# Kernel optimization log

Measured on AMD Instinct MI355X. Metric: run time of the kernel, lower is better.

## Reference

```python
import jax, jax.numpy as jnp
import numpy as np

GH = 256       # GRU hidden size
VOCAB = 1000
MAX_EP = 150
NPREV = NCURR = NNEXT = 64


def _gru_scan(emb, h0, wih, whh, bih, bhh):
    # torch nn.GRU single-layer math, scanned over the token axis
    H = h0.shape[0]
    def step(h, x_t):
        gi = wih @ x_t + bih            # [3H]
        gh = whh @ h + bhh              # [3H]
        r = jax.nn.sigmoid(gi[:H] + gh[:H])
        z = jax.nn.sigmoid(gi[H:2 * H] + gh[H:2 * H])
        n = jnp.tanh(gi[2 * H:] + r * gh[2 * H:])
        hn = (1.0 - z) * n + z * h
        return hn, hn
    _, hs = jax.lax.scan(step, h0, emb)
    return hs                            # [L, H]


def _conv(x, w, b, s):
    y = jax.lax.conv_general_dilated(x, w, (s, s), 'VALID',
                                     dimension_numbers=('NCHW', 'OIHW', 'NCHW'))
    return y + b[None, :, None, None]


def setup_inputs():
    key = jax.random.key(0)
    ks = jax.random.split(key, 48)
    f32 = jnp.float32
    def W(i, shape, s=0.05):
        return (jax.random.normal(ks[i], shape) * s).astype(f32)
    inp = dict(
        x=jax.random.normal(ks[0], (1, 3, 124, 124), f32),
        hx=jax.random.normal(ks[1], (1, 256), f32),
        cx=jax.random.normal(ks[2], (1, 256), f32),
        conv1_w=W(3, (128, 3, 8, 8)), conv1_b=jnp.zeros((128,), f32),
        conv2_w=W(4, (64, 128, 4, 4)), conv2_b=jnp.zeros((64,), f32),
        conv3_w=W(5, (64, 64, 4, 4)), conv3_b=jnp.zeros((64,), f32),
        emb_w=W(6, (VOCAB, 32), 1.0),
        gru_f_wih=W(7, (3 * GH, 32)), gru_f_whh=W(8, (3 * GH, GH)),
        gru_f_bih=jnp.zeros((3 * GH,), f32), gru_f_bhh=jnp.zeros((3 * GH,), f32),
        gru_b_wih=W(9, (3 * GH, 32)), gru_b_whh=W(10, (3 * GH, GH)),
        gru_b_bih=jnp.zeros((3 * GH,), f32), gru_b_bhh=jnp.zeros((3 * GH,), f32),
        time_emb_w=W(11, (MAX_EP + 1, 32), 1.0),
        temp_emb_w=W(12, (2, 32), 1.0),
        img_emb_w=W(13, (256, 64 * 6 * 6)), img_emb_b=jnp.zeros((256,), f32),
        attn_key_w=W(14, (256, 256 * 3)), attn_key_b=jnp.zeros((256,), f32),
        bilinear_A=W(15, (1, 256, 544)), bilinear_b=jnp.zeros((1,), f32),
        reduce_w=W(16, (128, 544)), reduce_b=jnp.zeros((128,), f32),
        gate_w=W(17, (64, 640)), gate_b=jnp.zeros((64,), f32),
        lin_w=W(18, (256, 64 * 6 * 6)), lin_b=jnp.zeros((256,), f32),
        lstm_wih=W(19, (1024, 256)), lstm_whh=W(20, (1024, 256)),
        lstm_bih=jnp.zeros((1024,), f32), lstm_bhh=jnp.zeros((1024,), f32),
        critic_w=W(21, (1, 288)), critic_b=jnp.zeros((1,), f32),
        actor_w=W(22, (4, 288)), actor_b=jnp.zeros((4,), f32),
        prev_inst=jax.random.randint(ks[23], (1, NPREV), 0, VOCAB),
        curr_inst=jax.random.randint(ks[24], (1, NCURR), 0, VOCAB),
        next_inst=jax.random.randint(ks[25], (1, NNEXT), 0, VOCAB),
        tx=jax.random.randint(ks[26], (1,), 0, MAX_EP + 1),
    )
    return inp


def reference(x, hx, cx, conv1_w, conv1_b, conv2_w, conv2_b, conv3_w, conv3_b,
              emb_w, gru_f_wih, gru_f_whh, gru_f_bih, gru_f_bhh,
              gru_b_wih, gru_b_whh, gru_b_bih, gru_b_bhh,
              time_emb_w, temp_emb_w, img_emb_w, img_emb_b,
              attn_key_w, attn_key_b, bilinear_A, bilinear_b,
              reduce_w, reduce_b, gate_w, gate_b, lin_w, lin_b,
              lstm_wih, lstm_whh, lstm_bih, lstm_bhh,
              critic_w, critic_b, actor_w, actor_b,
              prev_inst, curr_inst, next_inst, tx):
    np_, nc, nn_ = prev_inst.shape[1], curr_inst.shape[1], next_inst.shape[1]
    all_inst = jnp.concatenate([prev_inst, curr_inst, next_inst], axis=1)[0]  # [L]
    L = all_inst.shape[0]

    # CNN encoder
    h = jax.nn.relu(_conv(x, conv1_w, conv1_b, 4))
    h = jax.nn.relu(_conv(h, conv2_w, conv2_b, 2))
    x_img = jax.nn.relu(_conv(h, conv3_w, conv3_b, 2))       # [1,64,6,6]

    # token-looped GRUs -> single lax.scan each (note: original runs gru_b
    # over the SAME forward order then reverses the hidden list; replicated)
    emb = emb_w[all_inst]                                    # [L,32]
    h0 = jnp.zeros((GH,), emb.dtype)
    hs_f = _gru_scan(emb, h0, gru_f_wih, gru_f_whh, gru_f_bih, gru_f_bhh)
    hs_b = _gru_scan(emb, h0, gru_b_wih, gru_b_whh, gru_b_bih, gru_b_bhh)[::-1]
    curr_instr_rep = jnp.concatenate([hs_f[np_ + nc - 1], hs_b[np_]])[None]  # [1,512]
    ir_f = jnp.concatenate([hs_f[:np_], hs_f[L - nn_:]], axis=0)             # [M,256]
    ir_b = jnp.concatenate([hs_b[:np_], hs_b[L - nn_:]], axis=0)
    temp_tok = jnp.concatenate([jnp.zeros((np_,), jnp.int32), jnp.ones((nn_,), jnp.int32)])
    instr_rep = jnp.concatenate([ir_f, ir_b, temp_emb_w[temp_tok]], axis=1)  # [M,544]

    # bilinear attention over prev/next token states
    image_emb = x_img.reshape(1, -1) @ img_emb_w.T + img_emb_b               # [1,256]
    attn_key = jnp.concatenate([curr_instr_rep, image_emb], 1) @ attn_key_w.T + attn_key_b
    scores = jnp.einsum('k,okv,mv->mo', attn_key[0], bilinear_A, instr_rep) + bilinear_b  # [M,1]
    w = jax.nn.softmax(scores, axis=0)
    instr_sum = (instr_rep * w).sum(0, keepdims=True)                        # [1,544]

    # gating of image features
    gating = instr_sum @ reduce_w.T + reduce_b                               # [1,128]
    gate_key = jax.nn.sigmoid(jnp.concatenate([curr_instr_rep, gating], 1) @ gate_w.T + gate_b)  # [1,64]
    xg = (x_img * gate_key[:, :, None, None]).reshape(1, -1)
    z = jax.nn.relu(xg @ lin_w.T + lin_b)                                    # [1,256]

    # LSTMCell (torch gate order i,f,g,o)
    gates = z @ lstm_wih.T + lstm_bih + hx @ lstm_whh.T + lstm_bhh           # [1,1024]
    i, f, g, o = jnp.split(gates, 4, axis=1)
    cx2 = jax.nn.sigmoid(f) * cx + jax.nn.sigmoid(i) * jnp.tanh(g)
    hx2 = jax.nn.sigmoid(o) * jnp.tanh(cx2)

    feat = jnp.concatenate([hx2, time_emb_w[tx].reshape(-1, 32)], axis=1)    # [1,288]
    critic = feat @ critic_w.T + critic_b                                    # [1,1]
    actor = feat @ actor_w.T + actor_b                                       # [1,4]
    return critic, actor, hx2, cx2
```

## Files before the change

kernel.cpp:

```cpp
#include <hip/hip_runtime.h>
#include <hip/hip_bf16.h>

__device__ __forceinline__ float bf2f(unsigned short u) {
    unsigned int v = ((unsigned int)u) << 16;
    return __builtin_bit_cast(float, v);
}
__device__ __forceinline__ float sigm(float x) { return 1.0f / (1.0f + expf(-x)); }
__device__ __forceinline__ float san(float v) {
    return (v == v && fabsf(v) < 1e20f) ? v : 12345.0f;
}
__device__ __forceinline__ void wrout(void* out, int i, float v, int f32out) {
    if (f32out) ((float*)out)[i] = v;
    else ((__hip_bfloat16*)out)[i] = __float2bfloat16(v);
}
__device__ __forceinline__ int dot4(int a, int b, int c) {
#if __has_builtin(__builtin_amdgcn_sdot4)
    return __builtin_amdgcn_sdot4(a, b, c, false);
#else
    int d;
    asm("v_dot4_i32_i8 %0, %1, %2, %3" : "=v"(d) : "v"(a), "v"(b), "v"(c));
    return d;
#endif
}
__device__ __forceinline__ float fexp2(float x) {
#if __has_builtin(__builtin_amdgcn_exp2f)
    return __builtin_amdgcn_exp2f(x);
#else
    return exp2f(x);
#endif
}
__device__ __forceinline__ float frcp(float x) {
#if __has_builtin(__builtin_amdgcn_rcpf)
    return __builtin_amdgcn_rcpf(x);
#else
    return 1.0f / x;
#endif
}
__device__ __forceinline__ float fsigm(float x) {
    return frcp(1.0f + fexp2(x * -1.44269504f));
}
__device__ __forceinline__ float ftanh(float x) {
    float t = fexp2(x * 2.88539008f);
    return 1.0f - 2.0f * frcp(t + 1.0f);
}
__device__ __forceinline__ float wave_red(float acc) {
#pragma unroll
    for (int off = 32; off >= 1; off >>= 1) acc += __shfl_down(acc, off);
    return acc;
}
__device__ __forceinline__ int dpp_xor1(int a) {
    return __builtin_amdgcn_mov_dpp(a, 0xB1, 0xF, 0xF, true);
}
__device__ __forceinline__ int dpp_xor2(int a) {
    return __builtin_amdgcn_mov_dpp(a, 0x4E, 0xF, 0xF, true);
}

struct CanonArgs {
    const void* ptr[40];
    int start[41];
    int size[40];
};

__global__ void k_flag1000(void* out) {
    if (threadIdx.x == 0) ((unsigned int*)out)[0] = 0x447A0000u;
}

__global__ void k_detect_tokens(const void* x, int nx,
                                const int* __restrict__ prev, const int* __restrict__ curr,
                                const int* __restrict__ nxt, const int* __restrict__ tx,
                                float* __restrict__ flags, int* __restrict__ toks) {
    __shared__ float sm[256];
    __shared__ int sInt64;
    int tid = threadIdx.x;
    const unsigned short* xs = (const unsigned short*)x;
    float mx = 0.0f;
    for (int i = tid; i < nx; i += 256) {
        float f = bf2f(xs[i]);
        float a = (f == f) ? fabsf(f) : 1e30f;
        mx = fmaxf(mx, a);
    }
    sm[tid] = mx;
    __syncthreads();
    for (int s = 128; s >= 1; s >>= 1) {
        if (tid < s) sm[tid] = fmaxf(sm[tid], sm[tid + s]);
        __syncthreads();
    }
    if (tid == 0) {
        flags[0] = (sm[0] > 100.0f) ? 1.0f : 0.0f;
        int anyOdd = 0;
        for (int k = 0; k < 32; ++k) anyOdd |= curr[2 * k + 1];
        int i64 = (anyOdd == 0) ? 1 : 0;
        flags[1] = (float)i64;
        sInt64 = i64;
    }
    __syncthreads();
    int stride = sInt64 ? 2 : 1;
    if (tid < 192) {
        const int* src = (tid < 64) ? prev : ((tid < 128) ? curr : nxt);
        int v = src[(tid & 63) * stride];
        toks[tid] = min(max(v, 0), 999);
    }
    if (tid == 0) toks[192] = min(max(tx[0], 0), 150);
}

__global__ void k_convert(CanonArgs a, const float* __restrict__ flags,
                          float* __restrict__ C) {
    int base = blockIdx.x << 10;
    int t = 0;
    while (t < 39 && base >= a.start[t + 1]) ++t;
    int local = base - a.start[t] + (threadIdx.x << 2);
    int sz = a.size[t];
    float4 v = make_float4(0.0f, 0.0f, 0.0f, 0.0f);
    int f32in = (flags[0] != 0.0f);
    if (local + 3 < sz) {
        if (f32in) {
            v = *(const float4*)((const float*)a.ptr[t] + local);
        } else {
            uint2 u = *(const uint2*)((const unsigned short*)a.ptr[t] + local);
            v.x = bf2f((unsigned short)(u.x & 0xffff));
            v.y = bf2f((unsigned short)(u.x >> 16));
            v.z = bf2f((unsigned short)(u.y & 0xffff));
            v.w = bf2f((unsigned short)(u.y >> 16));
        }
    } else if (local < sz) {
        float tmp[4] = {0.0f, 0.0f, 0.0f, 0.0f};
        for (int q = 0; q < 4 && local + q < sz; ++q) {
            if (f32in) tmp[q] = ((const float*)a.ptr[t])[local + q];
            else tmp[q] = bf2f(((const unsigned short*)a.ptr[t])[local + q]);
        }
        v = make_float4(tmp[0], tmp[1], tmp[2], tmp[3]);
    }
    *(float4*)(C + base + (threadIdx.x << 2)) = v;
}

__global__ void k_conv1(const float* __restrict__ x, const float* __restrict__ w,
                        const float* __restrict__ b, float* __restrict__ out) {
    int idx = blockIdx.x * 256 + threadIdx.x;
    int oc = idx / 900;
    int rem = idx - oc * 900;
    int oh = rem / 30;
    int ow = rem - oh * 30;
    float acc = b[oc];
    for (int ic = 0; ic < 3; ++ic) {
        int xb = ic * 15376 + (oh * 4) * 124 + ow * 4;
        int wb = oc * 192 + ic * 64;
#pragma unroll
        for (int kh = 0; kh < 8; ++kh) {
            const float2* xr = (const float2*)(x + xb + kh * 124);
            const float2* wr = (const float2*)(w + wb + kh * 8);
#pragma unroll
            for (int p = 0; p < 4; ++p) {
                float2 xv = xr[p];
                float2 wv = wr[p];
                acc += xv.x * wv.x + xv.y * wv.y;
            }
        }
    }
    out[idx] = fmaxf(acc, 0.0f);
}

__global__ void k_conv2(const float* __restrict__ in, const float* __restrict__ w,
                        const float* __restrict__ b, float* __restrict__ out) {
    int wid = (blockIdx.x * 256 + threadIdx.x) >> 6;
    int lane = threadIdx.x & 63;
    int oc = wid / 196;
    int rem = wid - oc * 196;
    int oh = rem / 14, ow = rem - oh * 14;
    float acc = 0.0f;
#pragma unroll 8
    for (int i = 0; i < 32; ++i) {
        int e = lane + (i << 6);
        int ic = e >> 4, k = e & 15, kh = k >> 2, kw = k & 3;
        acc += in[ic * 900 + (oh * 2 + kh) * 30 + ow * 2 + kw] * w[oc * 2048 + e];
    }
    acc = wave_red(acc);
    if (lane == 0) out[wid] = fmaxf(acc + b[oc], 0.0f);
}

__global__ void k_conv3(const float* __restrict__ in, const float* __restrict__ w,
                        const float* __restrict__ b, float* __restrict__ out) {
    int wid = (blockIdx.x * 256 + threadIdx.x) >> 6;
    int lane = threadIdx.x & 63;
    int oc = wid / 36;
    int rem = wid - oc * 36;
    int oh = rem / 6, ow = rem - oh * 6;
    float acc = 0.0f;
#pragma unroll
    for (int i = 0; i < 16; ++i) {
        int e = lane + (i << 6);
        int ic = e >> 4, k = e & 15, kh = k >> 2, kw = k & 3;
        acc += in[ic * 196 + (oh * 2 + kh) * 14 + ow * 2 + kw] * w[oc * 1024 + e];
    }
    acc = wave_red(acc);
    if (lane == 0) out[wid] = fmaxf(acc + b[oc], 0.0f);
}

__global__ void k_imgemb(const float* __restrict__ ximg, const float* __restrict__ w,
                         const float* __restrict__ b, float* __restrict__ out) {
    int j = blockIdx.x;
    int t = threadIdx.x;
    const float* wr = w + j * 2304;
    float acc = 0.0f;
    for (int k = t; k < 2304; k += 64) acc += wr[k] * ximg[k];
    acc = wave_red(acc);
    if (t == 0) out[j] = acc + b[j];
}

__global__ void k_gi(const int* __restrict__ toks, const float* __restrict__ emb,
                     const float* __restrict__ wih_f, const float* __restrict__ bih_f,
                     const float* __restrict__ bhh_f,
                     const float* __restrict__ wih_b, const float* __restrict__ bih_b,
                     const float* __restrict__ bhh_b,
                     float* __restrict__ gi) {
    int t = blockIdx.y;
    int gru = blockIdx.z;
    int j = blockIdx.x * 256 + threadIdx.x;
    __shared__ float e[32];
    int tok = toks[t];
    if (threadIdx.x < 32) e[threadIdx.x] = emb[tok * 32 + threadIdx.x];
    __syncthreads();
    const float* wih = gru ? wih_b : wih_f;
    const float* bih = gru ? bih_b : bih_f;
    const float* bhh = gru ? bhh_b : bhh_f;
    const float2* wr = (const float2*)(wih + j * 32);
    float acc = bih[j] + ((j < 512) ? bhh[j] : 0.0f);
#pragma unroll
    for (int k = 0; k < 16; ++k) {
        float2 wv = wr[k];
        acc += wv.x * e[2 * k] + wv.y * e[2 * k + 1];
    }
    gi[(gru * 192 + t) * 768 + j] = acc;
}

__global__ __launch_bounds__(512, 1) void k_gru(
    const float* __restrict__ whh_f, const float* __restrict__ bhh_f,
    const float* __restrict__ whh_b, const float* __restrict__ bhh_b,
    const float* __restrict__ gi, float* __restrict__ hs) {
    __shared__ unsigned int hq[2][72];

    int gru = blockIdx.x;
    const float* whh = gru ? whh_b : whh_f;
    const float* bhh = gru ? bhh_b : bhh_f;
    const float* gib = gi + gru * 192 * 768;
    float* hso = hs + gru * 192 * 256;

    int t = threadIdx.x;
    int c = t & 3;
    int g = t >> 2;
    int j0 = g * 2;
    int d = c & 1;
    int jme = j0 + d;

    int wq[6][16];
    float inv6[6];
#pragma unroll
    for (int rl = 0; rl < 6; ++rl) {
        int sect = rl >> 1, dd = rl & 1;
        int row = sect * 256 + j0 + dd;
        const float4* src4 = (const float4*)(whh + row * 256 + c * 64);
        float mx = 0.0f;
#pragma unroll
        for (int q = 0; q < 16; ++q) {
            float4 f = src4[q];
            mx = fmaxf(mx, fmaxf(fmaxf(fabsf(f.x), fabsf(f.y)),
                                 fmaxf(fabsf(f.z), fabsf(f.w))));
        }
        mx = fmaxf(mx, __shfl_xor(mx, 1));
        mx = fmaxf(mx, __shfl_xor(mx, 2));
        float scale = 127.0f / fmaxf(mx, 1e-20f);
        inv6[rl] = mx * (1.0f / (127.0f * 127.0f));
#pragma unroll
        for (int q = 0; q < 16; ++q) {
            float4 f = src4[q];
            int p0 = (int)rintf(f.x * scale);
            int p1 = (int)rintf(f.y * scale);
            int p2 = (int)rintf(f.z * scale);
            int p3 = (int)rintf(f.w * scale);
            wq[rl][q] = (p0 & 0xff) | ((p1 & 0xff) << 8) | ((p2 & 0xff) << 16) | (p3 << 24);
        }
    }
    float invR = d ? inv6[1] : inv6[0];
    float invZ = d ? inv6[3] : inv6[2];
    float invN = d ? inv6[5] : inv6[4];
    float bhhn = bhh[512 + jme];

    if (t < 144) ((unsigned int*)hq)[t] = 0u;
    __syncthreads();

    float hprev = 0.0f;
    float cr0 = gib[jme],       cz0 = gib[256 + jme],       cn0 = gib[512 + jme];
    float cr1 = gib[768 + jme], cz1 = gib[1024 + jme],      cn1 = gib[1280 + jme];

    auto step = [&](const unsigned int* hbuf, unsigned int* hnxt, int S,
                    float gr, float gz, float gn) {
        const uint4* hp = (const uint4*)(hbuf + c * 16);
        uint4 hv0 = hp[0], hv1 = hp[1], hv2 = hp[2], hv3 = hp[3];
        int acc[6] = {0, 0, 0, 0, 0, 0};
#pragma unroll
        for (int rl = 0; rl < 6; ++rl) {
            acc[rl] = dot4(wq[rl][0],  (int)hv0.x, acc[rl]);
            acc[rl] = dot4(wq[rl][1],  (int)hv0.y, acc[rl]);
            acc[rl] = dot4(wq[rl][2],  (int)hv0.z, acc[rl]);
            acc[rl] = dot4(wq[rl][3],  (int)hv0.w, acc[rl]);
            acc[rl] = dot4(wq[rl][4],  (int)hv1.x, acc[rl]);
            acc[rl] = dot4(wq[rl][5],  (int)hv1.y, acc[rl]);
            acc[rl] = dot4(wq[rl][6],  (int)hv1.z, acc[rl]);
            acc[rl] = dot4(wq[rl][7],  (int)hv1.w, acc[rl]);
            acc[rl] = dot4(wq[rl][8],  (int)hv2.x, acc[rl]);
            acc[rl] = dot4(wq[rl][9],  (int)hv2.y, acc[rl]);
            acc[rl] = dot4(wq[rl][10], (int)hv2.z, acc[rl]);
            acc[rl] = dot4(wq[rl][11], (int)hv2.w, acc[rl]);
            acc[rl] = dot4(wq[rl][12], (int)hv3.x, acc[rl]);
            acc[rl] = dot4(wq[rl][13], (int)hv3.y, acc[rl]);
            acc[rl] = dot4(wq[rl][14], (int)hv3.z, acc[rl]);
            acc[rl] = dot4(wq[rl][15], (int)hv3.w, acc[rl]);
        }
#pragma unroll
        for (int rl = 0; rl < 6; ++rl) {
            acc[rl] += dpp_xor1(acc[rl]);
            acc[rl] += dpp_xor2(acc[rl]);
        }
        int ai_r = d ? acc[1] : acc[0];
        int ai_z = d ? acc[3] : acc[2];
        int ai_n = d ? acc[5] : acc[4];
        float ar = (float)ai_r * invR;
        float az = (float)ai_z * invZ;
        float an = (float)ai_n * invN;
        float r = fsigm(gr + ar);
        float z = fsigm(gz + az);
        float n = ftanh(gn + r * (an + bhhn));
        hprev = z * (hprev - n) + n;

        int hbits = __builtin_bit_cast(int, hprev);
        int hpart = dpp_xor1(hbits);
        int q = (int)rintf(hprev * 127.0f) & 0xff;
        int qpk = q | ((dpp_xor1(q) & 0xff) << 8);
        if (c == 0) {
            *(float2*)(hso + S * 256 + j0) =
                make_float2(hprev, __builtin_bit_cast(float, hpart));
            ((unsigned short*)hnxt)[g] = (unsigned short)qpk;
        }
        asm volatile("s_waitcnt lgkmcnt(0)" ::: "memory");
        __builtin_amdgcn_s_barrier();
    };

    for (int i = 0; i < 96; ++i) {
        int s0 = 2 * i;
        float nr0 = 0.0f, nz0 = 0.0f, nn0 = 0.0f;
        if (s0 + 2 < 192) {
            const float* gp = gib + (s0 + 2) * 768 + jme;
            nr0 = gp[0]; nz0 = gp[256]; nn0 = gp[512];
        }
        step(&hq[0][0], &hq[1][0], s0, cr0, cz0, cn0);

        int s1 = s0 + 1;
        float nr1 = 0.0f, nz1 = 0.0f, nn1 = 0.0f;
        if (s1 + 2 < 192) {
            const float* gp = gib + (s1 + 2) * 768 + jme;
            nr1 = gp[0]; nz1 = gp[256]; nn1 = gp[512];
        }
        step(&hq[1][0], &hq[0][0], s1, cr1, cz1, cn1);

        cr0 = nr0; cz0 = nz0; cn0 = nn0;
        cr1 = nr1; cz1 = nz1; cn1 = nn1;
    }
}

__device__ __forceinline__ float ir_val(int m, int v, const float* hsf, const float* hsb,
                                        const float* temp_emb) {
    if (v < 256) { int r = (m < 64) ? m : 64 + m; return hsf[r * 256 + v]; }
    if (v < 512) { int r = (m < 64) ? 191 - m : 127 - m; return hsb[r * 256 + v - 256]; }
    return temp_emb[(m >= 64) * 32 + (v - 512)];
}

__global__ void k_attnkey(const float* __restrict__ hs, const float* __restrict__ imgemb,
                          const float* __restrict__ w, const float* __restrict__ b,
                          float* __restrict__ ak) {
    int j = blockIdx.x;
    int t = threadIdx.x;
    const float* hsf127 = hs + 127 * 256;
    const float* hsb127 = hs + 192 * 256 + 127 * 256;
    const float* wr = w + j * 768;
    float acc = 0.0f;
    for (int k = t; k < 768; k += 64) {
        float v = (k < 256) ? hsf127[k] : ((k < 512) ? hsb127[k - 256] : imgemb[k - 512]);
        acc += wr[k] * v;
    }
    acc = wave_red(acc);
    if (t == 0) ak[j] = acc + b[j];
}

__global__ void k_bilin(const float* __restrict__ A, const float* __restrict__ ak,
                        float* __restrict__ tmp) {
    int v = blockIdx.x;
    int t = threadIdx.x;
    float acc = 0.0f;
#pragma unroll
    for (int k = t; k < 256; k += 64) acc += A[k * 544 + v] * ak[k];
    acc = wave_red(acc);
    if (t == 0) tmp[v] = acc;
}

__global__ __launch_bounds__(1024) void k_attnmid(
    const float* __restrict__ hs, const float* __restrict__ temp_emb_w,
    const float* __restrict__ tmpv, const float* __restrict__ bb,
    const float* __restrict__ reduce_w, const float* __restrict__ reduce_b,
    const float* __restrict__ gate_w, const float* __restrict__ gate_b,
    float* __restrict__ gk) {
    const int tid = threadIdx.x;
    const float* hsf = hs;
    const float* hsb = hs + 192 * 256;
    __shared__ float stmp[544], ssc[128], ssum[544], sred[1024], sgating[128], scr[512];

    if (tid < 256) {
        scr[tid] = hsf[127 * 256 + tid];
        scr[256 + tid] = hsb[127 * 256 + tid];
    }
    if (tid < 544) stmp[tid] = tmpv[tid];
    __syncthreads();

    {
        int m = tid >> 3, q = tid & 7;
        float acc = 0.0f;
        for (int v = q * 68; v < q * 68 + 68; ++v) acc += stmp[v] * ir_val(m, v, hsf, hsb, temp_emb_w);
        sred[tid] = acc;
    }
    __syncthreads();
    if (tid < 128) {
        float acc = bb[0];
        for (int q = 0; q < 8; ++q) acc += sred[tid * 8 + q];
        ssc[tid] = acc;
        sred[tid] = acc;
    }
    __syncthreads();
#pragma unroll
    for (int s2 = 64; s2 >= 1; s2 >>= 1) {
        if (tid < s2) sred[tid] = fmaxf(sred[tid], sred[tid + s2]);
        __syncthreads();
    }
    float mx = sred[0];
    __syncthreads();
    if (tid < 128) {
        float e = expf(ssc[tid] - mx);
        ssc[tid] = e;
        sred[tid] = e;
    }
    __syncthreads();
#pragma unroll
    for (int s2 = 64; s2 >= 1; s2 >>= 1) {
        if (tid < s2) sred[tid] += sred[tid + s2];
        __syncthreads();
    }
    float inv = 1.0f / sred[0];
    __syncthreads();
    if (tid < 128) ssc[tid] *= inv;
    __syncthreads();

    if (tid < 544) {
        float acc = 0.0f;
        for (int m = 0; m < 128; ++m) acc += ssc[m] * ir_val(m, tid, hsf, hsb, temp_emb_w);
        ssum[tid] = acc;
    }
    __syncthreads();

    {
        int j = tid >> 3, q = tid & 7;
        const float2* wr = (const float2*)(reduce_w + j * 544 + q * 68);
        float acc = 0.0f;
        for (int k = 0; k < 34; ++k) {
            float2 wv = wr[k];
            acc += wv.x * ssum[q * 68 + 2 * k] + wv.y * ssum[q * 68 + 2 * k + 1];
        }
        sred[tid] = acc;
    }
    __syncthreads();
    if (tid < 128) {
        float acc = reduce_b[tid];
        for (int q = 0; q < 8; ++q) acc += sred[tid * 8 + q];
        sgating[tid] = acc;
    }
    __syncthreads();

    {
        int j = tid >> 4, q = tid & 15;
        const float2* wr = (const float2*)(gate_w + j * 640 + q * 40);
        float acc = 0.0f;
        for (int k = 0; k < 20; ++k) {
            float2 wv = wr[k];
            int v0 = q * 40 + 2 * k;
            float a0 = (v0 < 512) ? scr[v0] : sgating[v0 - 512];
            float a1 = (v0 + 1 < 512) ? scr[v0 + 1] : sgating[v0 + 1 - 512];
            acc += wv.x * a0 + wv.y * a1;
        }
        sred[tid] = acc;
    }
    __syncthreads();
    if (tid < 64) {
        float acc = gate_b[tid];
        for (int q = 0; q < 16; ++q) acc += sred[tid * 16 + q];
        gk[tid] = sigm(acc);
    }
}

__global__ void k_lin(const float* __restrict__ ximg, const float* __restrict__ gk,
                      const float* __restrict__ w, const float* __restrict__ b,
                      float* __restrict__ z) {
    int j = blockIdx.x;
    int t = threadIdx.x;
    __shared__ float sgk[64];
    if (t < 64) sgk[t] = gk[t];
    __syncthreads();
    const float* wr = w + j * 2304;
    float acc = 0.0f;
    for (int k = t; k < 2304; k += 64) acc += wr[k] * ximg[k] * sgk[k / 36];
    acc = wave_red(acc);
    if (t == 0) z[j] = fmaxf(acc + b[j], 0.0f);
}

__global__ void k_lstm(const float* __restrict__ z, const float* __restrict__ hx,
                       const float* __restrict__ wih, const float* __restrict__ whh,
                       const float* __restrict__ bih, const float* __restrict__ bhh,
                       float* __restrict__ sg) {
    int j = blockIdx.x;
    int t = threadIdx.x;
    const float* wi = wih + j * 256;
    const float* wh = whh + j * 256;
    float acc = 0.0f;
#pragma unroll
    for (int k = t; k < 256; k += 64) acc += wi[k] * z[k] + wh[k] * hx[k];
    acc = wave_red(acc);
    if (t == 0) sg[j] = acc + bih[j] + bhh[j];
}

__global__ __launch_bounds__(1024) void k_final(
    const float* __restrict__ sgg, const float* __restrict__ cx,
    const float* __restrict__ time_emb_w, const int* __restrict__ toks,
    const float* __restrict__ critic_w, const float* __restrict__ critic_b,
    const float* __restrict__ actor_w, const float* __restrict__ actor_b,
    const float* __restrict__ flags, void* __restrict__ out) {
    const int tid = threadIdx.x;
    __shared__ float sfeat[288], shx2[256], scx2[256], stmp[544], sred[1024];

    if (tid < 256) {
        float ii = sgg[tid], ff = sgg[256 + tid], gg = sgg[512 + tid], oo = sgg[768 + tid];
        float c2 = sigm(ff) * cx[tid] + sigm(ii) * tanhf(gg);
        float h2 = sigm(oo) * tanhf(c2);
        scx2[tid] = c2;
        shx2[tid] = h2;
        sfeat[tid] = h2;
    }
    if (tid < 32) sfeat[256 + tid] = time_emb_w[toks[192] * 32 + tid];
    __syncthreads();

    if (tid < 512) stmp[tid] = (tid < 288) ? critic_w[tid] * sfeat[tid] : 0.0f;
    {
        int a = tid >> 8, k = tid & 255;
        float pa = actor_w[a * 288 + k] * sfeat[k];
        if (k < 32) pa += actor_w[a * 288 + 256 + k] * sfeat[256 + k];
        sred[tid] = pa;
    }
    __syncthreads();
#pragma unroll
    for (int s2 = 256; s2 >= 1; s2 >>= 1) {
        if (tid < s2) stmp[tid] += stmp[tid + s2];
        int k = tid & 255;
        if (s2 <= 128 && k < s2) sred[tid] += sred[tid + s2];
        __syncthreads();
    }

    int f32out = (flags[0] != 0.0f) ? 1 : 0;
    if (tid == 0) wrout(out, 0, san(stmp[0] + critic_b[0]), f32out);
    if (tid < 4) wrout(out, 1 + tid, san(sred[tid * 256] + actor_b[tid]), f32out);
    if (tid < 256) {
        wrout(out, 5 + tid, san(shx2[tid]), f32out);
        wrout(out, 261 + tid, san(scx2[tid]), f32out);
    }
}

extern "C" void kernel_launch(void* const* d_in, const int* in_sizes, int n_in,
                              void* d_out, int out_size, void* d_ws, size_t ws_size,
                              hipStream_t stream) {
    if (n_in != 44) return;

    CanonArgs ca;
    int acc = 0;
    for (int i = 0; i < 40; ++i) {
        ca.ptr[i] = d_in[i];
        ca.start[i] = acc;
        ca.size[i] = in_sizes[i];
        acc += (in_sizes[i] + 1023) & ~1023;
    }
    ca.start[40] = acc;
    const int T = acc;

    float* ws     = (float*)d_ws;
    float* flags  = ws;
    int*   toks   = (int*)(ws + 64);
    float* imgemb = ws + 320;
    float* C      = ws + 640;
    float* gi     = C + T;
    float* hs     = gi + 294912;
    float* aux    = hs + 98304;
    float* ak     = aux;
    float* tmpv   = aux + 256;
    float* gk     = aux + 928;
    float* zv     = aux + 992;
    float* sg     = aux + 1248;
    float* h1     = gi;
    float* h2     = h1 + 115200;
    float* ximg   = h2 + 12544;

    size_t need = (size_t)(640 + T + 294912 + 98304 + 2272) * 4;
    if (ws_size < need) {
        k_flag1000<<<1, 64, 0, stream>>>(d_out);
        return;
    }

    const int* prev = (const int*)d_in[40];
    const int* curr = (const int*)d_in[41];
    const int* nxt  = (const int*)d_in[42];
    const int* tx   = (const int*)d_in[43];

    k_detect_tokens<<<1, 256, 0, stream>>>(d_in[0], in_sizes[0], prev, curr, nxt, tx,
                                           flags, toks);
    k_convert<<<T >> 10, 256, 0, stream>>>(ca, flags, C);

#define CP(i) (C + ca.start[i])
    k_gi<<<dim3(3, 192, 2), 256, 0, stream>>>(toks, CP(9),
                                              CP(10), CP(12), CP(13),
                                              CP(14), CP(16), CP(17), gi);
    k_gru<<<2, 512, 0, stream>>>(CP(11), CP(13), CP(15), CP(17), gi, hs);
    k_conv1<<<450, 256, 0, stream>>>(CP(0), CP(3), CP(4), h1);
    k_conv2<<<3136, 256, 0, stream>>>(h1, CP(5), CP(6), h2);
    k_conv3<<<576, 256, 0, stream>>>(h2, CP(7), CP(8), ximg);
    k_imgemb<<<256, 64, 0, stream>>>(ximg, CP(20), CP(21), imgemb);
    k_attnkey<<<256, 64, 0, stream>>>(hs, imgemb, CP(22), CP(23), ak);
    k_bilin<<<544, 64, 0, stream>>>(CP(24), ak, tmpv);
    k_attnmid<<<1, 1024, 0, stream>>>(hs, CP(19), tmpv, CP(25),
                                      CP(26), CP(27), CP(28), CP(29), gk);
    k_lin<<<256, 64, 0, stream>>>(ximg, gk, CP(30), CP(31), zv);
    k_lstm<<<1024, 64, 0, stream>>>(zv, CP(1), CP(32), CP(33), CP(34), CP(35), sg);
    k_final<<<1, 1024, 0, stream>>>(sg, CP(2), CP(18), toks,
                                    CP(36), CP(37), CP(38), CP(39), flags, d_out);
#undef CP
}
```

Baseline: 509.3 us.

## Compute GRU recurrent matvec with int8 MFMA instead of dot4 plus DPP reductions

Replaces the per-lane v_dot4 int8 matvec and DPP cross-lane reductions in the sequential GRU kernel with v_mfma_i32_16x16x64_i8 instructions. Weights are quantized into MFMA A-fragments held in registers, and the int8 hidden state is broadcast as the B operand. Each lane selects its own output element from the accumulator fragment. This shortens the per-step critical path of the 192-step recurrence, at the cost of wasted MFMA columns, inline-asm hazard nops and a new register and thread mapping.

```diff
diff --git a/kernel.cpp b/kernel.cpp
--- a/kernel.cpp
+++ b/kernel.cpp
@@ -1,5 +1,7 @@
 #include <hip/hip_runtime.h>
 #include <hip/hip_bf16.h>
+
+typedef int int4v __attribute__((ext_vector_type(4)));
 
 __device__ __forceinline__ float bf2f(unsigned short u) {
     unsigned int v = ((unsigned int)u) << 16;
@@ -12,15 +14,6 @@
 __device__ __forceinline__ void wrout(void* out, int i, float v, int f32out) {
     if (f32out) ((float*)out)[i] = v;
     else ((__hip_bfloat16*)out)[i] = __float2bfloat16(v);
-}
-__device__ __forceinline__ int dot4(int a, int b, int c) {
-#if __has_builtin(__builtin_amdgcn_sdot4)
-    return __builtin_amdgcn_sdot4(a, b, c, false);
-#else
-    int d;
-    asm("v_dot4_i32_i8 %0, %1, %2, %3" : "=v"(d) : "v"(a), "v"(b), "v"(c));
-    return d;
-#endif
 }
 __device__ __forceinline__ float fexp2(float x) {
 #if __has_builtin(__builtin_amdgcn_exp2f)
@@ -48,11 +41,10 @@
     for (int off = 32; off >= 1; off >>= 1) acc += __shfl_down(acc, off);
     return acc;
 }
-__device__ __forceinline__ int dpp_xor1(int a) {
-    return __builtin_amdgcn_mov_dpp(a, 0xB1, 0xF, 0xF, true);
-}
-__device__ __forceinline__ int dpp_xor2(int a) {
-    return __builtin_amdgcn_mov_dpp(a, 0x4E, 0xF, 0xF, true);
+__device__ __forceinline__ int sel4(int4v v, int rg) {
+    int a = (rg & 1) ? v.y : v.x;
+    int b = (rg & 1) ? v.w : v.z;
+    return (rg & 2) ? b : a;
 }
 
 struct CanonArgs {
@@ -236,7 +228,8 @@
     const float* __restrict__ whh_f, const float* __restrict__ bhh_f,
     const float* __restrict__ whh_b, const float* __restrict__ bhh_b,
     const float* __restrict__ gi, float* __restrict__ hs) {
-    __shared__ unsigned int hq[2][72];
+    __shared__ unsigned int hq[2][64];
+    __shared__ float sc[768];
 
     int gru = blockIdx.x;
     const float* whh = gru ? whh_b : whh_f;
@@ -245,100 +238,131 @@
     float* hso = hs + gru * 192 * 256;
 
     int t = threadIdx.x;
-    int c = t & 3;
-    int g = t >> 2;
-    int j0 = g * 2;
-    int d = c & 1;
-    int jme = j0 + d;
-
-    int wq[6][16];
-    float inv6[6];
-#pragma unroll
-    for (int rl = 0; rl < 6; ++rl) {
-        int sect = rl >> 1, dd = rl & 1;
-        int row = sect * 256 + j0 + dd;
-        const float4* src4 = (const float4*)(whh + row * 256 + c * 64);
-        float mx = 0.0f;
-#pragma unroll
-        for (int q = 0; q < 16; ++q) {
-            float4 f = src4[q];
-            mx = fmaxf(mx, fmaxf(fmaxf(fabsf(f.x), fabsf(f.y)),
-                                 fmaxf(fabsf(f.z), fabsf(f.w))));
-        }
-        mx = fmaxf(mx, __shfl_xor(mx, 1));
-        mx = fmaxf(mx, __shfl_xor(mx, 2));
-        float scale = 127.0f / fmaxf(mx, 1e-20f);
-        inv6[rl] = mx * (1.0f / (127.0f * 127.0f));
-#pragma unroll
-        for (int q = 0; q < 16; ++q) {
-            float4 f = src4[q];
-            int p0 = (int)rintf(f.x * scale);
-            int p1 = (int)rintf(f.y * scale);
-            int p2 = (int)rintf(f.z * scale);
-            int p3 = (int)rintf(f.w * scale);
-            wq[rl][q] = (p0 & 0xff) | ((p1 & 0xff) << 8) | ((p2 & 0xff) << 16) | (p3 << 24);
-        }
-    }
-    float invR = d ? inv6[1] : inv6[0];
-    float invZ = d ? inv6[3] : inv6[2];
-    float invN = d ? inv6[5] : inv6[4];
-    float bhhn = bhh[512 + jme];
-
-    if (t < 144) ((unsigned int*)hq)[t] = 0u;
-    __syncthreads();
+    int l = t & 63;
+    int w = t >> 6;
+    int lg = l >> 4;
+    int lr = l & 15;
+    int e_sel = (l >> 2) & 1;
+    int rg = l & 3;
+    int j = 32 * w + 16 * e_sel + 4 * lg + rg;
+
+    int4v A[3][2][4];
+#pragma unroll
+    for (int s3 = 0; s3 < 3; ++s3) {
+#pragma unroll
+        for (int e = 0; e < 2; ++e) {
+            int r = s3 * 256 + 32 * w + 16 * e + lr;
+            const float* rowp = whh + r * 256;
+            float4 tmp[16];
+            float mx = 0.0f;
+#pragma unroll
+            for (int q = 0; q < 4; ++q) {
+#pragma unroll
+                for (int f = 0; f < 4; ++f) {
+                    float4 v = *(const float4*)(rowp + 64 * q + 16 * lg + 4 * f);
+                    tmp[q * 4 + f] = v;
+                    mx = fmaxf(mx, fmaxf(fmaxf(fabsf(v.x), fabsf(v.y)),
+                                         fmaxf(fabsf(v.z), fabsf(v.w))));
+                }
+            }
+            mx = fmaxf(mx, __shfl_xor(mx, 16));
+            mx = fmaxf(mx, __shfl_xor(mx, 32));
+            float scale = 127.0f / fmaxf(mx, 1e-20f);
+            if (lg == 0) sc[r] = mx * (1.0f / (127.0f * 127.0f));
+#pragma unroll
+            for (int q = 0; q < 4; ++q) {
+                int dw[4];
+#pragma unroll
+                for (int f = 0; f < 4; ++f) {
+                    float4 v = tmp[q * 4 + f];
+                    int p0 = (int)rintf(v.x * scale) & 0xff;
+                    int p1 = (int)rintf(v.y * scale) & 0xff;
+                    int p2 = (int)rintf(v.z * scale) & 0xff;
+                    int p3 = (int)rintf(v.w * scale);
+                    dw[f] = p0 | (p1 << 8) | (p2 << 16) | (p3 << 24);
+                }
+                A[s3][e][q] = (int4v){dw[0], dw[1], dw[2], dw[3]};
+            }
+        }
+    }
+    if (t < 128) ((unsigned int*)hq)[t] = 0u;
+    __syncthreads();
+
+    float invR = sc[j];
+    float invZ = sc[256 + j];
+    float invN = sc[512 + j];
+    float bhhn = bhh[512 + j];
+    int wr8 = ((l & 8) == 0);
 
     float hprev = 0.0f;
-    float cr0 = gib[jme],       cz0 = gib[256 + jme],       cn0 = gib[512 + jme];
-    float cr1 = gib[768 + jme], cz1 = gib[1024 + jme],      cn1 = gib[1280 + jme];
+    float cr0 = gib[j],       cz0 = gib[256 + j],  cn0 = gib[512 + j];
+    float cr1 = gib[768 + j], cz1 = gib[1024 + j], cn1 = gib[1280 + j];
+
+    int4v zero4 = (int4v){0, 0, 0, 0};
 
     auto step = [&](const unsigned int* hbuf, unsigned int* hnxt, int S,
                     float gr, float gz, float gn) {
-        const uint4* hp = (const uint4*)(hbuf + c * 16);
-        uint4 hv0 = hp[0], hv1 = hp[1], hv2 = hp[2], hv3 = hp[3];
-        int acc[6] = {0, 0, 0, 0, 0, 0};
-#pragma unroll
-        for (int rl = 0; rl < 6; ++rl) {
-            acc[rl] = dot4(wq[rl][0],  (int)hv0.x, acc[rl]);
-            acc[rl] = dot4(wq[rl][1],  (int)hv0.y, acc[rl]);
-            acc[rl] = dot4(wq[rl][2],  (int)hv0.z, acc[rl]);
-            acc[rl] = dot4(wq[rl][3],  (int)hv0.w, acc[rl]);
-            acc[rl] = dot4(wq[rl][4],  (int)hv1.x, acc[rl]);
-            acc[rl] = dot4(wq[rl][5],  (int)hv1.y, acc[rl]);
-            acc[rl] = dot4(wq[rl][6],  (int)hv1.z, acc[rl]);
-            acc[rl] = dot4(wq[rl][7],  (int)hv1.w, acc[rl]);
-            acc[rl] = dot4(wq[rl][8],  (int)hv2.x, acc[rl]);
-            acc[rl] = dot4(wq[rl][9],  (int)hv2.y, acc[rl]);
-            acc[rl] = dot4(wq[rl][10], (int)hv2.z, acc[rl]);
-            acc[rl] = dot4(wq[rl][11], (int)hv2.w, acc[rl]);
-            acc[rl] = dot4(wq[rl][12], (int)hv3.x, acc[rl]);
-            acc[rl] = dot4(wq[rl][13], (int)hv3.y, acc[rl]);
-            acc[rl] = dot4(wq[rl][14], (int)hv3.z, acc[rl]);
-            acc[rl] = dot4(wq[rl][15], (int)hv3.w, acc[rl]);
-        }
-#pragma unroll
-        for (int rl = 0; rl < 6; ++rl) {
-            acc[rl] += dpp_xor1(acc[rl]);
-            acc[rl] += dpp_xor2(acc[rl]);
-        }
-        int ai_r = d ? acc[1] : acc[0];
-        int ai_z = d ? acc[3] : acc[2];
-        int ai_n = d ? acc[5] : acc[4];
-        float ar = (float)ai_r * invR;
-        float az = (float)ai_z * invZ;
-        float an = (float)ai_n * invN;
+        const char* hb = (const char*)hbuf;
+        int4v B0 = *(const int4v*)(hb + 16 * lg);
+        int4v B1 = *(const int4v*)(hb + 64 + 16 * lg);
+        int4v B2 = *(const int4v*)(hb + 128 + 16 * lg);
+        int4v B3 = *(const int4v*)(hb + 192 + 16 * lg);
+
+        int4v C00, C01, C10, C11, C20, C21;
+        asm volatile(
+            "v_mfma_i32_16x16x64_i8 %0, %7,  %31, %6\n\t"
+            "v_mfma_i32_16x16x64_i8 %1, %11, %31, %6\n\t"
+            "v_mfma_i32_16x16x64_i8 %2, %15, %31, %6\n\t"
+            "v_mfma_i32_16x16x64_i8 %3, %19, %31, %6\n\t"
+            "v_mfma_i32_16x16x64_i8 %4, %23, %31, %6\n\t"
+            "v_mfma_i32_16x16x64_i8 %5, %27, %31, %6\n\t"
+            "v_mfma_i32_16x16x64_i8 %0, %8,  %32, %0\n\t"
+            "v_mfma_i32_16x16x64_i8 %1, %12, %32, %1\n\t"
+            "v_mfma_i32_16x16x64_i8 %2, %16, %32, %2\n\t"
+            "v_mfma_i32_16x16x64_i8 %3, %20, %32, %3\n\t"
+            "v_mfma_i32_16x16x64_i8 %4, %24, %32, %4\n\t"
+            "v_mfma_i32_16x16x64_i8 %5, %28, %32, %5\n\t"
+            "v_mfma_i32_16x16x64_i8 %0, %9,  %33, %0\n\t"
+            "v_mfma_i32_16x16x64_i8 %1, %13, %33, %1\n\t"
+            "v_mfma_i32_16x16x64_i8 %2, %17, %33, %2\n\t"
+            "v_mfma_i32_16x16x64_i8 %3, %21, %33, %3\n\t"
+            "v_mfma_i32_16x16x64_i8 %4, %25, %33, %4\n\t"
+            "v_mfma_i32_16x16x64_i8 %5, %29, %33, %5\n\t"
+            "v_mfma_i32_16x16x64_i8 %0, %10, %34, %0\n\t"
+            "v_mfma_i32_16x16x64_i8 %1, %14, %34, %1\n\t"
+            "v_mfma_i32_16x16x64_i8 %2, %18, %34, %2\n\t"
+            "v_mfma_i32_16x16x64_i8 %3, %22, %34, %3\n\t"
+            "v_mfma_i32_16x16x64_i8 %4, %26, %34, %4\n\t"
+            "v_mfma_i32_16x16x64_i8 %5, %30, %34, %5\n\t"
+            "s_nop 7\n\t"
+            "s_nop 7"
+            : "=&v"(C00), "=&v"(C01), "=&v"(C10),
+              "=&v"(C11), "=&v"(C20), "=&v"(C21)
+            : "v"(zero4),
+              "v"(A[0][0][0]), "v"(A[0][0][1]), "v"(A[0][0][2]), "v"(A[0][0][3]),
+              "v"(A[0][1][0]), "v"(A[0][1][1]), "v"(A[0][1][2]), "v"(A[0][1][3]),
+              "v"(A[1][0][0]), "v"(A[1][0][1]), "v"(A[1][0][2]), "v"(A[1][0][3]),
+              "v"(A[1][1][0]), "v"(A[1][1][1]), "v"(A[1][1][2]), "v"(A[1][1][3]),
+              "v"(A[2][0][0]), "v"(A[2][0][1]), "v"(A[2][0][2]), "v"(A[2][0][3]),
+              "v"(A[2][1][0]), "v"(A[2][1][1]), "v"(A[2][1][2]), "v"(A[2][1][3]),
+              "v"(B0), "v"(B1), "v"(B2), "v"(B3));
+        __builtin_amdgcn_sched_barrier(0);
+
+        int ri = sel4(e_sel ? C01 : C00, rg);
+        int zi = sel4(e_sel ? C11 : C10, rg);
+        int ni = sel4(e_sel ? C21 : C20, rg);
+        float ar = (float)ri * invR;
+        float az = (float)zi * invZ;
+        float an = (float)ni * invN;
         float r = fsigm(gr + ar);
         float z = fsigm(gz + az);
         float n = ftanh(gn + r * (an + bhhn));
         hprev = z * (hprev - n) + n;
 
-        int hbits = __builtin_bit_cast(int, hprev);
-        int hpart = dpp_xor1(hbits);
-        int q = (int)rintf(hprev * 127.0f) & 0xff;
-        int qpk = q | ((dpp_xor1(q) & 0xff) << 8);
-        if (c == 0) {
-            *(float2*)(hso + S * 256 + j0) =
-                make_float2(hprev, __builtin_bit_cast(float, hpart));
-            ((unsigned short*)hnxt)[g] = (unsigned short)qpk;
+        int qv = (int)rintf(hprev * 127.0f);
+        if (wr8) {
+            hso[S * 256 + j] = hprev;
+            ((char*)hnxt)[j] = (char)qv;
         }
         asm volatile("s_waitcnt lgkmcnt(0)" ::: "memory");
         __builtin_amdgcn_s_barrier();
@@ -348,7 +372,7 @@
         int s0 = 2 * i;
         float nr0 = 0.0f, nz0 = 0.0f, nn0 = 0.0f;
         if (s0 + 2 < 192) {
-            const float* gp = gib + (s0 + 2) * 768 + jme;
+            const float* gp = gib + (s0 + 2) * 768 + j;
             nr0 = gp[0]; nz0 = gp[256]; nn0 = gp[512];
         }
         step(&hq[0][0], &hq[1][0], s0, cr0, cz0, cn0);
@@ -356,7 +380,7 @@
         int s1 = s0 + 1;
         float nr1 = 0.0f, nz1 = 0.0f, nn1 = 0.0f;
         if (s1 + 2 < 192) {
-            const float* gp = gib + (s1 + 2) * 768 + jme;
+            const float* gp = gib + (s1 + 2) * 768 + j;
             nr1 = gp[0]; nz1 = gp[256]; nn1 = gp[512];
         }
         step(&hq[1][0], &hq[0][0], s1, cr1, cz1, cn1);
```

Result: faster. 482.8 us (-5.2%).
